# Performance work log

Measured on AMD Instinct MI355X. Metric: run time of the kernel, lower is better.

The kernel has to match this reference:

```python
import jax, jax.numpy as jnp
import numpy as np

TH = 0.01  # threshold from init
H = 56
W = 56


def setup_inputs() -> dict:
    key = jax.random.key(0)
    k1, k2 = jax.random.split(key)
    x = jax.random.uniform(k1, (32, 512, 56, 56), dtype=jnp.float32)
    conv_w = jax.random.normal(k2, (512, 1, 1, 1), dtype=jnp.float32)
    scale = jnp.ones((1,), dtype=jnp.float32)
    wf = jnp.ones((1,), dtype=jnp.float32)
    return {"x": x, "conv_w": conv_w, "scale": scale, "wf": wf}


def reference(x, conv_w, scale, wf):
    B, C, _, _ = x.shape
    # per-channel spatial mean: alpha[b,c] = sum_hw x / (H*W)
    alpha = jnp.sum(x, axis=(2, 3)) / (H * W)  # [B, C]
    # channel-weighted spatial sum, averaged over channels -> saliency [B, H, W]
    sal = jnp.einsum('bchw,bc->bhw', x, alpha) / C
    # conv1x1 with 1 input channel: broadcastmul by per-output-channel scalar
    w = conv_w.reshape(1, -1, 1, 1)                 # [1, Cout, 1, 1]
    fm = sal[:, None, :, :] * w                     # [B, Cout, H, W]
    fm = jax.nn.relu(fm)
    fm = jnp.where(fm > TH, fm, 0.0)                # nn.Threshold(th, 0)
    return 1.0 - wf * jax.nn.sigmoid(scale * fm)
```

## Files before the change

### kernel.cpp

```cpp
#include <hip/hip_runtime.h>
#include <hip/hip_bf16.h>

#define B 32
#define C 512
#define HW 3136
#define HW4 784
#define TH 0.01f
#define NPG 32
#define CPB 16

typedef float fx4 __attribute__((ext_vector_type(4)));

__global__ __launch_bounds__(256, 4) void partial_kernel(const float* __restrict__ x,
                                                         float* __restrict__ out) {
    const int b  = blockIdx.y;
    const int pg = blockIdx.x;
    const int t  = threadIdx.x;
    const int l  = t & 63;
    const int wv = t >> 6;

    __shared__ float sums[2][2][4];

    const float* __restrict__ xb = x + (size_t)b * C * HW;
    const int qbase = wv * 196;

    fx4 acc0 = (fx4)0.f, acc1 = (fx4)0.f, acc2 = (fx4)0.f, acc3 = (fx4)0.f;

    #pragma unroll 2
    for (int g = 0; g < 8; ++g) {
        const int c0 = pg * CPB + 2 * g;
        const fx4* __restrict__ p0 = (const fx4*)(xb + (size_t)c0 * HW) + qbase + l;
        const fx4* __restrict__ p1 = (const fx4*)(xb + (size_t)(c0 + 1) * HW) + qbase + l;

        const fx4 a0 = p0[0], a1 = p0[64], a2 = p0[128];
        const fx4 b0 = p1[0], b1 = p1[64], b2 = p1[128];
        fx4 a3 = (fx4)0.f, b3 = (fx4)0.f;
        if (l < 4) { a3 = p0[192]; b3 = p1[192]; }

        float sa = (((a0.x + a0.y) + (a0.z + a0.w)) + ((a1.x + a1.y) + (a1.z + a1.w))) +
                   (((a2.x + a2.y) + (a2.z + a2.w)) + ((a3.x + a3.y) + (a3.z + a3.w)));
        float sb = (((b0.x + b0.y) + (b0.z + b0.w)) + ((b1.x + b1.y) + (b1.z + b1.w))) +
                   (((b2.x + b2.y) + (b2.z + b2.w)) + ((b3.x + b3.y) + (b3.z + b3.w)));
        #pragma unroll
        for (int off = 1; off < 64; off <<= 1) {
            sa += __shfl_xor(sa, off);
            sb += __shfl_xor(sb, off);
        }
        if (l == 0) {
            sums[g & 1][0][wv] = sa;
            sums[g & 1][1][wv] = sb;
        }
        __syncthreads();
        const float al0 = ((sums[g & 1][0][0] + sums[g & 1][0][1]) +
                           (sums[g & 1][0][2] + sums[g & 1][0][3])) * (1.0f / (float)HW);
        const float al1 = ((sums[g & 1][1][0] + sums[g & 1][1][1]) +
                           (sums[g & 1][1][2] + sums[g & 1][1][3])) * (1.0f / (float)HW);

        acc0 += a0 * al0 + b0 * al1;
        acc1 += a1 * al0 + b1 * al1;
        acc2 += a2 * al0 + b2 * al1;
        acc3 += a3 * al0 + b3 * al1;
    }

    fx4* __restrict__ dst = (fx4*)(out + (size_t)b * C * HW + (size_t)pg * HW) + qbase + l;
    dst[0]   = acc0;
    dst[64]  = acc1;
    dst[128] = acc2;
    if (l < 4) dst[192] = acc3;
}

__global__ __launch_bounds__(256) void out_kernel(const float* __restrict__ w,
                                                  const float* __restrict__ scale_p,
                                                  const float* __restrict__ wf_p,
                                                  float* __restrict__ out) {
    const int b    = blockIdx.y;
    const int tile = blockIdx.x;
    const int t    = threadIdx.x;
    const int hw4  = t & 15;
    const int pg2  = t >> 4;
    const int lane = t & 63;
    const int wid  = t >> 6;

    const fx4* __restrict__ P =
        (const fx4*)(out + (size_t)b * C * HW) + tile * 16 + hw4;
    fx4 s = P[(size_t)(2 * pg2) * HW4] + P[(size_t)(2 * pg2 + 1) * HW4];

    s.x += __shfl_xor(s.x, 16); s.y += __shfl_xor(s.y, 16);
    s.z += __shfl_xor(s.z, 16); s.w += __shfl_xor(s.w, 16);
    s.x += __shfl_xor(s.x, 32); s.y += __shfl_xor(s.y, 32);
    s.z += __shfl_xor(s.z, 32); s.w += __shfl_xor(s.w, 32);

    __shared__ fx4 red[4][16];
    if (lane < 16) red[wid][lane] = s;
    __syncthreads();

    __shared__ fx4 sal_sm[16];
    if (t < 16) {
        sal_sm[t] = ((red[0][t] + red[1][t]) + (red[2][t] + red[3][t])) *
                    (1.0f / (float)C);
    }
    __syncthreads();

    const float scale = scale_p[0];
    const float wf    = wf_p[0];
    const float out_zero = 1.0f - 0.5f * wf;
    const fx4 s4 = sal_sm[hw4];

    fx4* __restrict__ ob = (fx4*)(out + (size_t)b * C * HW) + tile * 16 + hw4;
    const int c0 = pg2 * 32;

    #pragma unroll 4
    for (int k = 0; k < 32; ++k) {
        const int co = c0 + k;
        const float wc = w[co];
        fx4 r;
        float fm;
        fm = s4.x * wc;
        r.x = (fm > TH) ? 1.0f - wf / (1.0f + __expf(-scale * fm)) : out_zero;
        fm = s4.y * wc;
        r.y = (fm > TH) ? 1.0f - wf / (1.0f + __expf(-scale * fm)) : out_zero;
        fm = s4.z * wc;
        r.z = (fm > TH) ? 1.0f - wf / (1.0f + __expf(-scale * fm)) : out_zero;
        fm = s4.w * wc;
        r.w = (fm > TH) ? 1.0f - wf / (1.0f + __expf(-scale * fm)) : out_zero;
        __builtin_nontemporal_store(r, ob + (size_t)co * HW4);
    }
}

extern "C" void kernel_launch(void* const* d_in, const int* in_sizes, int n_in,
                              void* d_out, int out_size, void* d_ws, size_t ws_size,
                              hipStream_t stream) {
    const float* x      = (const float*)d_in[0];
    const float* conv_w = (const float*)d_in[1];
    const float* scale  = (const float*)d_in[2];
    const float* wf     = (const float*)d_in[3];
    float* out = (float*)d_out;

    dim3 gridA(NPG, B);
    partial_kernel<<<gridA, 256, 0, stream>>>(x, out);

    dim3 gridB(HW4 / 16, B);
    out_kernel<<<gridB, 256, 0, stream>>>(conv_w, scale, wf, out);
}
```

Measured before the change: 82.90 us.

## Reduce partials in last-arriving block and stream contiguous output chunks

```diff
diff --git a/kernel.cpp b/kernel.cpp
--- a/kernel.cpp
+++ b/kernel.cpp
@@ -8,11 +8,17 @@
 #define TH 0.01f
 #define NPG 32
 #define CPB 16
+#define FX4_PER_B (C * HW4)
+#define BLK_B 56
+#define FX4_PER_BLK (FX4_PER_B / BLK_B)
+#define ITERS (FX4_PER_BLK / 256)
 
 typedef float fx4 __attribute__((ext_vector_type(4)));
 
 __global__ __launch_bounds__(256, 4) void partial_kernel(const float* __restrict__ x,
-                                                         float* __restrict__ out) {
+                                                         float* __restrict__ out,
+                                                         float* __restrict__ sal,
+                                                         int* __restrict__ cnt) {
     const int b  = blockIdx.y;
     const int pg = blockIdx.x;
     const int t  = threadIdx.x;
@@ -20,6 +26,7 @@
     const int wv = t >> 6;
 
     __shared__ float sums[2][2][4];
+    __shared__ int sh_last;
 
     const float* __restrict__ xb = x + (size_t)b * C * HW;
     const int qbase = wv * 196;
@@ -67,63 +74,75 @@
     dst[64]  = acc1;
     dst[128] = acc2;
     if (l < 4) dst[192] = acc3;
+
+    __syncthreads();
+    if (t == 0) {
+        __threadfence();
+        const int old = __hip_atomic_fetch_add(&cnt[b], 1, __ATOMIC_ACQ_REL,
+                                               __HIP_MEMORY_SCOPE_AGENT);
+        sh_last = (old == NPG - 1);
+    }
+    __syncthreads();
+    if (!sh_last) return;
+
+    const fx4* __restrict__ Pb = (const fx4*)(out + (size_t)b * C * HW);
+    fx4* __restrict__ salv = (fx4*)(sal + (size_t)b * HW);
+    for (int i = t; i < HW4; i += 256) {
+        fx4 s = (fx4)0.f;
+        #pragma unroll
+        for (int g = 0; g < NPG; ++g) s += Pb[(size_t)g * HW4 + i];
+        salv[i] = s * (1.0f / (float)C);
+    }
 }
 
-__global__ __launch_bounds__(256) void out_kernel(const float* __restrict__ w,
+__global__ __launch_bounds__(256) void out_kernel(const fx4* __restrict__ sal,
+                                                  const float* __restrict__ w,
                                                   const float* __restrict__ scale_p,
                                                   const float* __restrict__ wf_p,
                                                   float* __restrict__ out) {
-    const int b    = blockIdx.y;
-    const int tile = blockIdx.x;
-    const int t    = threadIdx.x;
-    const int hw4  = t & 15;
-    const int pg2  = t >> 4;
-    const int lane = t & 63;
-    const int wid  = t >> 6;
+    const int bid = blockIdx.x;
+    const int b   = bid / BLK_B;
+    const int j   = bid % BLK_B;
+    const int t   = threadIdx.x;
 
-    const fx4* __restrict__ P =
-        (const fx4*)(out + (size_t)b * C * HW) + tile * 16 + hw4;
-    fx4 s = P[(size_t)(2 * pg2) * HW4] + P[(size_t)(2 * pg2 + 1) * HW4];
-
-    s.x += __shfl_xor(s.x, 16); s.y += __shfl_xor(s.y, 16);
-    s.z += __shfl_xor(s.z, 16); s.w += __shfl_xor(s.w, 16);
-    s.x += __shfl_xor(s.x, 32); s.y += __shfl_xor(s.y, 32);
-    s.z += __shfl_xor(s.z, 32); s.w += __shfl_xor(s.w, 32);
-
-    __shared__ fx4 red[4][16];
-    if (lane < 16) red[wid][lane] = s;
-    __syncthreads();
-
-    __shared__ fx4 sal_sm[16];
-    if (t < 16) {
-        sal_sm[t] = ((red[0][t] + red[1][t]) + (red[2][t] + red[3][t])) *
-                    (1.0f / (float)C);
-    }
+    __shared__ fx4  sal_sm[HW4];
+    __shared__ float w_sm[C];
+    const fx4* __restrict__ sb = sal + (size_t)b * HW4;
+    for (int i = t; i < HW4; i += 256) sal_sm[i] = sb[i];
+    for (int i = t; i < C;   i += 256) w_sm[i]  = w[i];
     __syncthreads();
 
     const float scale = scale_p[0];
     const float wf    = wf_p[0];
-    const float out_zero = 1.0f - 0.5f * wf;
-    const fx4 s4 = sal_sm[hw4];
+    const float z     = 1.0f - 0.5f * wf;
 
-    fx4* __restrict__ ob = (fx4*)(out + (size_t)b * C * HW) + tile * 16 + hw4;
-    const int c0 = pg2 * 32;
+    const int F0 = j * FX4_PER_BLK;
+    fx4* __restrict__ ob = (fx4*)(out + (size_t)b * C * HW) + F0;
 
-    #pragma unroll 4
-    for (int k = 0; k < 32; ++k) {
-        const int co = c0 + k;
-        const float wc = w[co];
+    int colb = F0 % HW4;
+    int cob  = F0 / HW4;
+
+    for (int it = 0; it < ITERS; ++it) {
+        int c = colb + t;
+        const int wrapped = (c >= HW4) ? 1 : 0;
+        c -= wrapped ? HW4 : 0;
+        const fx4  s4 = sal_sm[c];
+        const float wc = w_sm[cob + wrapped];
+
         fx4 r;
         float fm;
         fm = s4.x * wc;
-        r.x = (fm > TH) ? 1.0f - wf / (1.0f + __expf(-scale * fm)) : out_zero;
+        r.x = (fm > TH) ? 1.0f - wf / (1.0f + __expf(-scale * fm)) : z;
         fm = s4.y * wc;
-        r.y = (fm > TH) ? 1.0f - wf / (1.0f + __expf(-scale * fm)) : out_zero;
+        r.y = (fm > TH) ? 1.0f - wf / (1.0f + __expf(-scale * fm)) : z;
         fm = s4.z * wc;
-        r.z = (fm > TH) ? 1.0f - wf / (1.0f + __expf(-scale * fm)) : out_zero;
+        r.z = (fm > TH) ? 1.0f - wf / (1.0f + __expf(-scale * fm)) : z;
         fm = s4.w * wc;
-        r.w = (fm > TH) ? 1.0f - wf / (1.0f + __expf(-scale * fm)) : out_zero;
-        __builtin_nontemporal_store(r, ob + (size_t)co * HW4);
+        r.w = (fm > TH) ? 1.0f - wf / (1.0f + __expf(-scale * fm)) : z;
+        __builtin_nontemporal_store(r, ob + it * 256 + t);
+
+        colb += 256;
+        if (colb >= HW4) { colb -= HW4; ++cob; }
     }
 }
 
@@ -135,10 +154,13 @@
     const float* scale  = (const float*)d_in[2];
     const float* wf     = (const float*)d_in[3];
     float* out = (float*)d_out;
+    float* sal = (float*)d_ws;
+    int*   cnt = (int*)((char*)d_ws + (size_t)B * HW * 4);
+
+    hipMemsetAsync(cnt, 0, B * sizeof(int), stream);
 
     dim3 gridA(NPG, B);
-    partial_kernel<<<gridA, 256, 0, stream>>>(x, out);
+    partial_kernel<<<gridA, 256, 0, stream>>>(x, out, sal, cnt);
 
-    dim3 gridB(HW4 / 16, B);
-    out_kernel<<<gridB, 256, 0, stream>>>(conv_w, scale, wf, out);
+    out_kernel<<<B * BLK_B, 256, 0, stream>>>((const fx4*)sal, conv_w, scale, wf, out);
 }
```

After: 163.6 us. 97.3% more time.

## Double-buffer channel-pair loads in partial kernel and use lighter barrier

Applied to the files above, without the earlier changes.

```diff
diff --git a/kernel.cpp b/kernel.cpp
--- a/kernel.cpp
+++ b/kernel.cpp
@@ -26,21 +26,42 @@
 
     fx4 acc0 = (fx4)0.f, acc1 = (fx4)0.f, acc2 = (fx4)0.f, acc3 = (fx4)0.f;
 
-    #pragma unroll 2
+    fx4 A0[4], B0[4], A1[4], B1[4];
+
+    {
+        const fx4* __restrict__ p0 = (const fx4*)(xb + (size_t)(pg * CPB) * HW) + qbase + l;
+        const fx4* __restrict__ p1 = (const fx4*)(xb + (size_t)(pg * CPB + 1) * HW) + qbase + l;
+        A0[0] = p0[0]; A0[1] = p0[64]; A0[2] = p0[128];
+        B0[0] = p1[0]; B0[1] = p1[64]; B0[2] = p1[128];
+        A0[3] = (fx4)0.f; B0[3] = (fx4)0.f;
+        if (l < 4) { A0[3] = p0[192]; B0[3] = p1[192]; }
+    }
+
+    #pragma unroll
     for (int g = 0; g < 8; ++g) {
-        const int c0 = pg * CPB + 2 * g;
-        const fx4* __restrict__ p0 = (const fx4*)(xb + (size_t)c0 * HW) + qbase + l;
-        const fx4* __restrict__ p1 = (const fx4*)(xb + (size_t)(c0 + 1) * HW) + qbase + l;
+        fx4* Ac = (g & 1) ? A1 : A0;
+        fx4* Bc = (g & 1) ? B1 : B0;
+        fx4* An = (g & 1) ? A0 : A1;
+        fx4* Bn = (g & 1) ? B0 : B1;
 
-        const fx4 a0 = p0[0], a1 = p0[64], a2 = p0[128];
-        const fx4 b0 = p1[0], b1 = p1[64], b2 = p1[128];
-        fx4 a3 = (fx4)0.f, b3 = (fx4)0.f;
-        if (l < 4) { a3 = p0[192]; b3 = p1[192]; }
+        if (g < 7) {
+            const int c0 = pg * CPB + 2 * (g + 1);
+            const fx4* __restrict__ p0 = (const fx4*)(xb + (size_t)c0 * HW) + qbase + l;
+            const fx4* __restrict__ p1 = (const fx4*)(xb + (size_t)(c0 + 1) * HW) + qbase + l;
+            An[0] = p0[0]; An[1] = p0[64]; An[2] = p0[128];
+            Bn[0] = p1[0]; Bn[1] = p1[64]; Bn[2] = p1[128];
+            An[3] = (fx4)0.f; Bn[3] = (fx4)0.f;
+            if (l < 4) { An[3] = p0[192]; Bn[3] = p1[192]; }
+        }
 
-        float sa = (((a0.x + a0.y) + (a0.z + a0.w)) + ((a1.x + a1.y) + (a1.z + a1.w))) +
-                   (((a2.x + a2.y) + (a2.z + a2.w)) + ((a3.x + a3.y) + (a3.z + a3.w)));
-        float sb = (((b0.x + b0.y) + (b0.z + b0.w)) + ((b1.x + b1.y) + (b1.z + b1.w))) +
-                   (((b2.x + b2.y) + (b2.z + b2.w)) + ((b3.x + b3.y) + (b3.z + b3.w)));
+        float sa = (((Ac[0].x + Ac[0].y) + (Ac[0].z + Ac[0].w)) +
+                    ((Ac[1].x + Ac[1].y) + (Ac[1].z + Ac[1].w))) +
+                   (((Ac[2].x + Ac[2].y) + (Ac[2].z + Ac[2].w)) +
+                    ((Ac[3].x + Ac[3].y) + (Ac[3].z + Ac[3].w)));
+        float sb = (((Bc[0].x + Bc[0].y) + (Bc[0].z + Bc[0].w)) +
+                    ((Bc[1].x + Bc[1].y) + (Bc[1].z + Bc[1].w))) +
+                   (((Bc[2].x + Bc[2].y) + (Bc[2].z + Bc[2].w)) +
+                    ((Bc[3].x + Bc[3].y) + (Bc[3].z + Bc[3].w)));
         #pragma unroll
         for (int off = 1; off < 64; off <<= 1) {
             sa += __shfl_xor(sa, off);
@@ -50,16 +71,20 @@
             sums[g & 1][0][wv] = sa;
             sums[g & 1][1][wv] = sb;
         }
-        __syncthreads();
+        asm volatile("s_waitcnt lgkmcnt(0)" ::: "memory");
+        __builtin_amdgcn_sched_barrier(0);
+        __builtin_amdgcn_s_barrier();
+        __builtin_amdgcn_sched_barrier(0);
+
         const float al0 = ((sums[g & 1][0][0] + sums[g & 1][0][1]) +
                            (sums[g & 1][0][2] + sums[g & 1][0][3])) * (1.0f / (float)HW);
         const float al1 = ((sums[g & 1][1][0] + sums[g & 1][1][1]) +
                            (sums[g & 1][1][2] + sums[g & 1][1][3])) * (1.0f / (float)HW);
 
-        acc0 += a0 * al0 + b0 * al1;
-        acc1 += a1 * al0 + b1 * al1;
-        acc2 += a2 * al0 + b2 * al1;
-        acc3 += a3 * al0 + b3 * al1;
+        acc0 += Ac[0] * al0 + Bc[0] * al1;
+        acc1 += Ac[1] * al0 + Bc[1] * al1;
+        acc2 += Ac[2] * al0 + Bc[2] * al1;
+        acc3 += Ac[3] * al0 + Bc[3] * al1;
     }
 
     fx4* __restrict__ dst = (fx4*)(out + (size_t)b * C * HW + (size_t)pg * HW) + qbase + l;
```

After: 190.5 us. 2.3x slower.
